# Optimization experiments

Measured on AMD Instinct MI355X. Metric: run time of the kernel, lower is better.

The kernel has to match this reference:

```python
import jax, jax.numpy as jnp
import numpy as np

EPS = 1e-9  # Dice BatchNormalization epsilon


def dice(x, alpha):
    # Keras BatchNormalization(axis=-1, center=False, scale=False) in training
    # mode: normalize over all axes except the last using batch statistics.
    mean = jnp.mean(x, axis=(0, 1), keepdims=True)
    var = jnp.var(x, axis=(0, 1), keepdims=True)
    x_normed = (x - mean) * jax.lax.rsqrt(var + EPS)
    p = jax.nn.sigmoid(x_normed)
    return alpha * (1.0 - p) * x + p * x


def setup_inputs() -> dict:
    key = jax.random.key(0)
    ks = jax.random.split(key, 11)
    B, T, D = 512, 2048, 20
    keys_ = jax.random.normal(ks[0], (B, T, D), dtype=jnp.float32)
    query = jax.random.normal(ks[1], (B, 1, D), dtype=jnp.float32)
    mask = jax.random.randint(ks[2], (B, T), 0, 2) > 0
    # DNN tower weights: hidden dims 80 -> 32 -> 16, attention head 16 -> 1
    W0 = jax.random.normal(ks[3], (80, 32), dtype=jnp.float32) * 0.1
    b0 = jax.random.normal(ks[4], (32,), dtype=jnp.float32) * 0.1
    a0 = jax.random.normal(ks[5], (32,), dtype=jnp.float32) * 0.1
    W1 = jax.random.normal(ks[6], (32, 16), dtype=jnp.float32) * 0.1
    b1 = jax.random.normal(ks[7], (16,), dtype=jnp.float32) * 0.1
    a1 = jax.random.normal(ks[8], (16,), dtype=jnp.float32) * 0.1
    wk = jax.random.normal(ks[9], (16, 1), dtype=jnp.float32) * 0.1
    bk = jax.random.normal(ks[10], (1,), dtype=jnp.float32) * 0.1
    return {"keys": keys_, "query": query, "mask": mask,
            "W0": W0, "b0": b0, "a0": a0,
            "W1": W1, "b1": b1, "a1": a1,
            "wk": wk, "bk": bk}


def reference(keys, query, mask, W0, b0, a0, W1, b1, a1, wk, bk):
    B, T, D = keys.shape
    # repeat query along the key/time axis: [B,1,D] -> [B,T,D]
    queries = jnp.broadcast_to(query, (B, T, D))
    # local-activation features: [B,T,4D] = [B,T,80]
    att = jnp.concatenate([queries, keys, queries - keys, queries * keys], axis=-1)
    # DNN tower with Dice activations (dropout is identity at inference)
    h = dice(att @ W0 + b0, a0)   # [B,T,32]
    h = dice(h @ W1 + b1, a1)     # [B,T,16]
    score = h @ wk + bk           # [B,T,1]
    outputs = jnp.transpose(score, (0, 2, 1))  # [B,1,T]
    # NOTE: the original code computes the masked scores into self.outputs but
    # then (weight_normalization=False, return_score=False) overwrites it with
    # matmul(outputs, keys) using the UNMASKED scores -- we reproduce that.
    return jnp.matmul(outputs, keys)  # [B,1,D]
```

## Files before the change

kernel.cpp:

```cpp
#include <hip/hip_runtime.h>
#include <hip/hip_cooperative_groups.h>

namespace cg = cooperative_groups;


#define BB 512
#define TT 2048
#define DD 20
#define C0 32
#define C1 16

#define NTH 256
#define NPOS 4
#define POSB (NTH * NPOS)
#define NROUND (TT / POSB)
#define NSLOT 8

#define WS_P1 0
#define WS_P2 512
#define WS_ZERO_N 768
#define WS_BLOB 896
#define BLOB_J 24
#define BLOB_B (C0 * BLOB_J)

#define PIN(x) asm volatile("" : "+v"(x))
#define AGLOAD(p) \
    __hip_atomic_load((p), __ATOMIC_RELAXED, __HIP_MEMORY_SCOPE_AGENT)

__device__ __forceinline__ float fast_sigmoid(float x) {
    return __builtin_amdgcn_rcpf(1.0f + __expf(-x));
}

__device__ __forceinline__ void load_krow(const float* __restrict__ row,
                                          float* kk) {
    const float4* kr = (const float4*)row;
    float4 a = kr[0], b = kr[1], c = kr[2], d = kr[3], e = kr[4];
    kk[0] = a.x; kk[1] = a.y; kk[2] = a.z; kk[3] = a.w;
    kk[4] = b.x; kk[5] = b.y; kk[6] = b.z; kk[7] = b.w;
    kk[8] = c.x; kk[9] = c.y; kk[10] = c.z; kk[11] = c.w;
    kk[12] = d.x; kk[13] = d.y; kk[14] = d.z; kk[15] = d.w;
    kk[16] = e.x; kk[17] = e.y; kk[18] = e.z; kk[19] = e.w;
}

__global__ void prep_kernel(const float* __restrict__ query,
                            const float* __restrict__ W0,
                            const float* __restrict__ b0,
                            float* __restrict__ blob) {
    const int b = blockIdx.x * 2 + (threadIdx.x >> 5);
    const int j = threadIdx.x & 31;
    float cj = b0[j];
    float* dst = blob + (size_t)b * BLOB_B + j * BLOB_J;
#pragma unroll
    for (int d = 0; d < DD; ++d) {
        float w_q = W0[d * C0 + j];
        float w_k = W0[(DD + d) * C0 + j];
        float w_d = W0[(2 * DD + d) * C0 + j];
        float w_p = W0[(3 * DD + d) * C0 + j];
        float qd = query[b * DD + d];
        dst[d] = w_k - w_d + qd * w_p;
        cj = fmaf(qd, w_q + w_d, cj);
    }
    dst[20] = cj;
}

#define LOAD_AND_PIN_KEYS(r)                                                 \
    float kk[NPOS][DD];                                                      \
    _Pragma("unroll") for (int pp = 0; pp < NPOS; ++pp)                      \
        load_krow(kbase + (size_t)((r)*POSB + tid + pp * NTH) * DD, kk[pp]); \
    _Pragma("unroll") for (int pp = 0; pp < NPOS; ++pp)                      \
        _Pragma("unroll") for (int d = 0; d < DD; ++d) PIN(kk[pp][d]);

#define TOWER_JLOOP()                                                        \
    _Pragma("unroll 1") for (int j = 0; j < C0; ++j) {                       \
        const float* wr = bA + j * BLOB_J;                                   \
        const float* ur = W1 + j * C1;                                       \
        const float cj = wr[20];                                             \
        const float2 ss = lss0[j];                                           \
        const float al = a0[j];                                              \
        const float nal = 1.0f - al;                                         \
        float h[NPOS];                                                       \
        _Pragma("unroll") for (int pp = 0; pp < NPOS; ++pp) {                \
            float hh = cj;                                                   \
            _Pragma("unroll") for (int d = 0; d < DD; ++d)                   \
                hh = fmaf(kk[pp][d], wr[d], hh);                             \
            h[pp] = hh;                                                      \
        }                                                                    \
        _Pragma("unroll") for (int pp = 0; pp < NPOS; ++pp) {                \
            float pr = fast_sigmoid(fmaf(h[pp], ss.x, ss.y));                \
            float h0d = h[pp] * fmaf(pr, nal, al);                           \
            _Pragma("unroll") for (int c = 0; c < C1; ++c)                   \
                h1[pp][c] = fmaf(h0d, ur[c], h1[pp][c]);                     \
        }                                                                    \
    }

__device__ __forceinline__ void phase1_body(int b, int tid, int lane,
                                            const float* __restrict__ bA,
                                            const float* __restrict__ kbase,
                                            float* __restrict__ ws) {
    float s[C0], q[C0];
#pragma unroll
    for (int j = 0; j < C0; ++j) { s[j] = 0.f; q[j] = 0.f; }
#pragma unroll 1
    for (int r = 0; r < NROUND; ++r) {
        LOAD_AND_PIN_KEYS(r)
#pragma unroll
        for (int j = 0; j < C0; ++j) {
            const float* wr = bA + j * BLOB_J;
            const float cj = wr[20];
            float sv = 0.f, qv = 0.f;
#pragma unroll
            for (int pp = 0; pp < NPOS; ++pp) {
                float hh = cj;
#pragma unroll
                for (int d = 0; d < DD; ++d) hh = fmaf(kk[pp][d], wr[d], hh);
                sv += hh;
                qv = fmaf(hh, hh, qv);
            }
            s[j] += sv;
            q[j] += qv;
        }
    }
    float redv = 0.f;
#pragma unroll
    for (int v = 0; v < 2 * C0; ++v) {
        float val = (v < C0) ? s[v] : q[v - C0];
#pragma unroll
        for (int o = 32; o >= 1; o >>= 1) val += __shfl_xor(val, o);
        if (lane == v) redv = val;
    }
    atomicAdd(&ws[WS_P1 + (b & (NSLOT - 1)) * (2 * C0) + lane], redv);
}

__device__ __forceinline__ void finalize0(int tid, float* __restrict__ ws,
                                          float2* __restrict__ lss0) {
    if (tid < C0) {
        float sv = 0.f, qv = 0.f;
#pragma unroll
        for (int k = 0; k < NSLOT; ++k) {
            sv += AGLOAD(&ws[WS_P1 + k * (2 * C0) + tid]);
            qv += AGLOAD(&ws[WS_P1 + k * (2 * C0) + C0 + tid]);
        }
        const float invN = 1.0f / (float)(BB * TT);
        float mean = sv * invN;
        float var = qv * invN - mean * mean;
        float sc = rsqrtf(var + 1e-9f);
        lss0[tid] = make_float2(sc, -mean * sc);
    }
}

__device__ __forceinline__ void phase2_body(
    int b, int tid, int lane, const float* __restrict__ bA,
    const float* __restrict__ kbase, const float* __restrict__ a0,
    const float* __restrict__ W1, const float* __restrict__ b1,
    const float2* __restrict__ lss0, float* __restrict__ ws) {
    float s1[C1], q1[C1];
#pragma unroll
    for (int c = 0; c < C1; ++c) { s1[c] = 0.f; q1[c] = 0.f; }
#pragma unroll 1
    for (int r = 0; r < NROUND; ++r) {
        LOAD_AND_PIN_KEYS(r)
        float h1[NPOS][C1];
#pragma unroll
        for (int pp = 0; pp < NPOS; ++pp)
#pragma unroll
            for (int c = 0; c < C1; ++c) h1[pp][c] = 0.f;
        TOWER_JLOOP()
#pragma unroll
        for (int c = 0; c < C1; ++c) {
            float bc = b1[c];
#pragma unroll
            for (int pp = 0; pp < NPOS; ++pp) {
                float v = h1[pp][c] + bc;
                s1[c] += v;
                q1[c] = fmaf(v, v, q1[c]);
            }
        }
    }
    float redv = 0.f;
#pragma unroll
    for (int v = 0; v < 2 * C1; ++v) {
        float val = (v < C1) ? s1[v] : q1[v - C1];
#pragma unroll
        for (int o = 32; o >= 1; o >>= 1) val += __shfl_xor(val, o);
        if (lane == v) redv = val;
    }
    if (lane < 2 * C1)
        atomicAdd(&ws[WS_P2 + (b & (NSLOT - 1)) * (2 * C1) + lane], redv);
}

__device__ __forceinline__ void finalize1(int tid, float* __restrict__ ws,
                                          const float* __restrict__ a1,
                                          const float* __restrict__ wk,
                                          float4* __restrict__ ld1v) {
    if (tid < C1) {
        float sv = 0.f, qv = 0.f;
#pragma unroll
        for (int k = 0; k < NSLOT; ++k) {
            sv += AGLOAD(&ws[WS_P2 + k * (2 * C1) + tid]);
            qv += AGLOAD(&ws[WS_P2 + k * (2 * C1) + C1 + tid]);
        }
        const float invN = 1.0f / (float)(BB * TT);
        float mean = sv * invN;
        float var = qv * invN - mean * mean;
        float sc = rsqrtf(var + 1e-9f);
        ld1v[tid] = make_float4(sc, -mean * sc, a1[tid], wk[tid]);
    }
}

__device__ __forceinline__ void phase3_body(
    int b, int tid, int lane, int wave, const float* __restrict__ bA,
    const float* __restrict__ kbase, const float* __restrict__ a0,
    const float* __restrict__ W1, const float* __restrict__ b1,
    const float* __restrict__ bk, const float2* __restrict__ lss0,
    const float4* __restrict__ ld1v, float (*red)[DD],
    float* __restrict__ out) {
    const float bkv = bk[0];
    float oacc[DD];
#pragma unroll
    for (int d = 0; d < DD; ++d) oacc[d] = 0.f;
#pragma unroll 1
    for (int r = 0; r < NROUND; ++r) {
        LOAD_AND_PIN_KEYS(r)
        float h1[NPOS][C1];
#pragma unroll
        for (int pp = 0; pp < NPOS; ++pp)
#pragma unroll
            for (int c = 0; c < C1; ++c) h1[pp][c] = 0.f;
        TOWER_JLOOP()
#pragma unroll
        for (int pp = 0; pp < NPOS; ++pp) {
            float score = bkv;
#pragma unroll
            for (int c = 0; c < C1; ++c) {
                float v = h1[pp][c] + b1[c];
                float4 dv = ld1v[c];
                float pr = fast_sigmoid(fmaf(v, dv.x, dv.y));
                float hd = v * fmaf(pr, 1.0f - dv.z, dv.z);
                score = fmaf(hd, dv.w, score);
            }
#pragma unroll
            for (int d = 0; d < DD; ++d)
                oacc[d] = fmaf(score, kk[pp][d], oacc[d]);
        }
    }
    float redv = 0.f;
#pragma unroll
    for (int v = 0; v < DD; ++v) {
        float val = oacc[v];
#pragma unroll
        for (int o = 32; o >= 1; o >>= 1) val += __shfl_xor(val, o);
        if (lane == v) redv = val;
    }
    if (lane < DD) red[wave][lane] = redv;
    __syncthreads();
    if (tid < DD)
        out[b * DD + tid] =
            red[0][tid] + red[1][tid] + red[2][tid] + red[3][tid];
}

__global__ __launch_bounds__(NTH, 2) void fused_kernel(
    const float* __restrict__ keys, const float* __restrict__ blob,
    const float* __restrict__ a0, const float* __restrict__ W1,
    const float* __restrict__ b1, const float* __restrict__ a1,
    const float* __restrict__ wk, const float* __restrict__ bk,
    float* __restrict__ ws, float* __restrict__ out) {
    const int b = blockIdx.x;
    const int tid = threadIdx.x, wave = tid >> 6, lane = tid & 63;
    const float* bA = blob + (size_t)b * BLOB_B;
    const float* kbase = keys + (size_t)b * TT * DD;

    __shared__ float2 lss0[C0];
    __shared__ float4 ld1v[C1];
    __shared__ float red[4][DD];

    phase1_body(b, tid, lane, bA, kbase, ws);
    cg::this_grid().sync();
    finalize0(tid, ws, lss0);
    __syncthreads();
    phase2_body(b, tid, lane, bA, kbase, a0, W1, b1, lss0, ws);
    cg::this_grid().sync();
    finalize1(tid, ws, a1, wk, ld1v);
    __syncthreads();
    phase3_body(b, tid, lane, wave, bA, kbase, a0, W1, b1, bk, lss0, ld1v,
                red, out);
}

__global__ __launch_bounds__(NTH, 2) void pass1_kernel(
    const float* __restrict__ keys, const float* __restrict__ blob,
    float* __restrict__ ws) {
    const int b = blockIdx.x;
    const int tid = threadIdx.x, lane = tid & 63;
    phase1_body(b, tid, lane, blob + (size_t)b * BLOB_B,
                keys + (size_t)b * TT * DD, ws);
}

__global__ __launch_bounds__(NTH, 2) void pass2_kernel(
    const float* __restrict__ keys, const float* __restrict__ blob,
    const float* __restrict__ a0, const float* __restrict__ W1,
    const float* __restrict__ b1, float* __restrict__ ws) {
    const int b = blockIdx.x;
    const int tid = threadIdx.x, lane = tid & 63;
    __shared__ float2 lss0[C0];
    finalize0(tid, ws, lss0);
    __syncthreads();
    phase2_body(b, tid, lane, blob + (size_t)b * BLOB_B,
                keys + (size_t)b * TT * DD, a0, W1, b1, lss0, ws);
}

__global__ __launch_bounds__(NTH, 2) void pass3_kernel(
    const float* __restrict__ keys, const float* __restrict__ blob,
    const float* __restrict__ a0, const float* __restrict__ W1,
    const float* __restrict__ b1, const float* __restrict__ a1,
    const float* __restrict__ wk, const float* __restrict__ bk,
    float* __restrict__ ws, float* __restrict__ out) {
    const int b = blockIdx.x;
    const int tid = threadIdx.x, wave = tid >> 6, lane = tid & 63;
    __shared__ float2 lss0[C0];
    __shared__ float4 ld1v[C1];
    __shared__ float red[4][DD];
    finalize0(tid, ws, lss0);
    finalize1(tid, ws, a1, wk, ld1v);
    __syncthreads();
    phase3_body(b, tid, lane, wave, blob + (size_t)b * BLOB_B,
                keys + (size_t)b * TT * DD, a0, W1, b1, bk, lss0, ld1v, red,
                out);
}

extern "C" void kernel_launch(void* const* d_in, const int* in_sizes, int n_in,
                              void* d_out, int out_size, void* d_ws,
                              size_t ws_size, hipStream_t stream) {
    const float* keys = (const float*)d_in[0];
    const float* query = (const float*)d_in[1];
    const float* W0 = (const float*)d_in[3];
    const float* b0 = (const float*)d_in[4];
    const float* a0 = (const float*)d_in[5];
    const float* W1 = (const float*)d_in[6];
    const float* b1 = (const float*)d_in[7];
    const float* a1 = (const float*)d_in[8];
    const float* wk = (const float*)d_in[9];
    const float* bk = (const float*)d_in[10];
    float* out = (float*)d_out;
    float* ws = (float*)d_ws;
    float* blob = ws + WS_BLOB;
    const float* blobc = blob;

    hipMemsetAsync(ws, 0, WS_ZERO_N * sizeof(float), stream);
    prep_kernel<<<BB / 2, 64, 0, stream>>>(query, W0, b0, blob);

    static int use_coop = -1;
    if (use_coop < 0) {
        int nb = 0, ncu = 0;
        hipError_t e1 = hipOccupancyMaxActiveBlocksPerMultiprocessor(
            &nb, (const void*)fused_kernel, NTH, 0);
        hipDeviceProp_t prop;
        hipError_t e2 = hipGetDeviceProperties(&prop, 0);
        if (e2 == hipSuccess) ncu = prop.multiProcessorCount;
        use_coop = (e1 == hipSuccess && e2 == hipSuccess && nb * ncu >= BB)
                       ? 1
                       : 0;
    }

    if (use_coop) {
        void* args[] = {(void*)&keys, (void*)&blobc, (void*)&a0, (void*)&W1,
                        (void*)&b1,   (void*)&a1,    (void*)&wk, (void*)&bk,
                        (void*)&ws,   (void*)&out};
        hipError_t e = hipLaunchCooperativeKernel(
            (const void*)fused_kernel, dim3(BB), dim3(NTH), args, 0, stream);
        if (e != hipSuccess) use_coop = 0;
    }
    if (!use_coop) {
        pass1_kernel<<<BB, NTH, 0, stream>>>(keys, blob, ws);
        pass2_kernel<<<BB, NTH, 0, stream>>>(keys, blob, a0, W1, b1, ws);
        pass3_kernel<<<BB, NTH, 0, stream>>>(keys, blob, a0, W1, b1, a1, wk,
                                             bk, ws, out);
    }
}
```

Measured before the change: 274.0 us.

## Split each batch across two blocks and raise occupancy to four blocks per CU

Each batch row's 2048 time steps are now split into two 1024-step chunks handled by separate blocks. The grid doubles, per-thread positions drop from 4 to 2, and launch bounds go from 2 to 4 blocks per CU. Because two blocks now contribute to each output row, the final write becomes an atomicAdd. Zeroing of the output and workspace moves into the prep kernel in place of the separate memset. The goal is more concurrent waves to hide memory latency and a lighter register load per thread. The cost is more atomics, a larger cooperative grid to synchronise, and tighter register limits that could cause spills.

```diff
diff --git a/kernel.cpp b/kernel.cpp
--- a/kernel.cpp
+++ b/kernel.cpp
@@ -11,9 +11,12 @@
 #define C1 16
 
 #define NTH 256
-#define NPOS 4
+#define NPOS 2
 #define POSB (NTH * NPOS)
-#define NROUND (TT / POSB)
+#define CHUNK 1024
+#define NROUND (CHUNK / POSB)
+#define NBLK (TT / CHUNK)
+#define GRID (BB * NBLK)
 #define NSLOT 8
 
 #define WS_P1 0
@@ -45,9 +48,14 @@
 __global__ void prep_kernel(const float* __restrict__ query,
                             const float* __restrict__ W0,
                             const float* __restrict__ b0,
-                            float* __restrict__ blob) {
+                            float* __restrict__ blob, float* __restrict__ ws,
+                            float* __restrict__ out) {
     const int b = blockIdx.x * 2 + (threadIdx.x >> 5);
     const int j = threadIdx.x & 31;
+    if (blockIdx.x == 0) {
+        for (int i = threadIdx.x; i < WS_ZERO_N; i += 64) ws[i] = 0.f;
+    }
+    if (j < DD) out[b * DD + j] = 0.f;
     float cj = b0[j];
     float* dst = blob + (size_t)b * BLOB_B + j * BLOB_J;
 #pragma unroll
@@ -93,7 +101,7 @@
         }                                                                    \
     }
 
-__device__ __forceinline__ void phase1_body(int b, int tid, int lane,
+__device__ __forceinline__ void phase1_body(int slot, int tid, int lane,
                                             const float* __restrict__ bA,
                                             const float* __restrict__ kbase,
                                             float* __restrict__ ws) {
@@ -128,7 +136,7 @@
         for (int o = 32; o >= 1; o >>= 1) val += __shfl_xor(val, o);
         if (lane == v) redv = val;
     }
-    atomicAdd(&ws[WS_P1 + (b & (NSLOT - 1)) * (2 * C0) + lane], redv);
+    atomicAdd(&ws[WS_P1 + slot * (2 * C0) + lane], redv);
 }
 
 __device__ __forceinline__ void finalize0(int tid, float* __restrict__ ws,
@@ -149,7 +157,7 @@
 }
 
 __device__ __forceinline__ void phase2_body(
-    int b, int tid, int lane, const float* __restrict__ bA,
+    int slot, int tid, int lane, const float* __restrict__ bA,
     const float* __restrict__ kbase, const float* __restrict__ a0,
     const float* __restrict__ W1, const float* __restrict__ b1,
     const float2* __restrict__ lss0, float* __restrict__ ws) {
@@ -185,7 +193,7 @@
         if (lane == v) redv = val;
     }
     if (lane < 2 * C1)
-        atomicAdd(&ws[WS_P2 + (b & (NSLOT - 1)) * (2 * C1) + lane], redv);
+        atomicAdd(&ws[WS_P2 + slot * (2 * C1) + lane], redv);
 }
 
 __device__ __forceinline__ void finalize1(int tid, float* __restrict__ ws,
@@ -208,7 +216,7 @@
 }
 
 __device__ __forceinline__ void phase3_body(
-    int b, int tid, int lane, int wave, const float* __restrict__ bA,
+    int batch, int tid, int lane, int wave, const float* __restrict__ bA,
     const float* __restrict__ kbase, const float* __restrict__ a0,
     const float* __restrict__ W1, const float* __restrict__ b1,
     const float* __restrict__ bk, const float2* __restrict__ lss0,
@@ -254,66 +262,70 @@
     if (lane < DD) red[wave][lane] = redv;
     __syncthreads();
     if (tid < DD)
-        out[b * DD + tid] =
-            red[0][tid] + red[1][tid] + red[2][tid] + red[3][tid];
-}
-
-__global__ __launch_bounds__(NTH, 2) void fused_kernel(
+        atomicAdd(&out[batch * DD + tid],
+                  red[0][tid] + red[1][tid] + red[2][tid] + red[3][tid]);
+}
+
+__global__ __launch_bounds__(NTH, 4) void fused_kernel(
     const float* __restrict__ keys, const float* __restrict__ blob,
     const float* __restrict__ a0, const float* __restrict__ W1,
     const float* __restrict__ b1, const float* __restrict__ a1,
     const float* __restrict__ wk, const float* __restrict__ bk,
     float* __restrict__ ws, float* __restrict__ out) {
-    const int b = blockIdx.x;
+    const int batch = blockIdx.x >> 1, chunk = blockIdx.x & 1;
+    const int slot = blockIdx.x & (NSLOT - 1);
     const int tid = threadIdx.x, wave = tid >> 6, lane = tid & 63;
-    const float* bA = blob + (size_t)b * BLOB_B;
-    const float* kbase = keys + (size_t)b * TT * DD;
+    const float* bA = blob + (size_t)batch * BLOB_B;
+    const float* kbase = keys + ((size_t)batch * TT + chunk * CHUNK) * DD;
 
     __shared__ float2 lss0[C0];
     __shared__ float4 ld1v[C1];
     __shared__ float red[4][DD];
 
-    phase1_body(b, tid, lane, bA, kbase, ws);
+    phase1_body(slot, tid, lane, bA, kbase, ws);
     cg::this_grid().sync();
     finalize0(tid, ws, lss0);
     __syncthreads();
-    phase2_body(b, tid, lane, bA, kbase, a0, W1, b1, lss0, ws);
+    phase2_body(slot, tid, lane, bA, kbase, a0, W1, b1, lss0, ws);
     cg::this_grid().sync();
     finalize1(tid, ws, a1, wk, ld1v);
     __syncthreads();
-    phase3_body(b, tid, lane, wave, bA, kbase, a0, W1, b1, bk, lss0, ld1v,
-                red, out);
-}
-
-__global__ __launch_bounds__(NTH, 2) void pass1_kernel(
+    phase3_body(batch, tid, lane, wave, bA, kbase, a0, W1, b1, bk, lss0,
+                ld1v, red, out);
+}
+
+__global__ __launch_bounds__(NTH, 4) void pass1_kernel(
     const float* __restrict__ keys, const float* __restrict__ blob,
     float* __restrict__ ws) {
-    const int b = blockIdx.x;
+    const int batch = blockIdx.x >> 1, chunk = blockIdx.x & 1;
     const int tid = threadIdx.x, lane = tid & 63;
-    phase1_body(b, tid, lane, blob + (size_t)b * BLOB_B,
-                keys + (size_t)b * TT * DD, ws);
-}
-
-__global__ __launch_bounds__(NTH, 2) void pass2_kernel(
+    phase1_body(blockIdx.x & (NSLOT - 1), tid, lane,
+                blob + (size_t)batch * BLOB_B,
+                keys + ((size_t)batch * TT + chunk * CHUNK) * DD, ws);
+}
+
+__global__ __launch_bounds__(NTH, 4) void pass2_kernel(
     const float* __restrict__ keys, const float* __restrict__ blob,
     const float* __restrict__ a0, const float* __restrict__ W1,
     const float* __restrict__ b1, float* __restrict__ ws) {
-    const int b = blockIdx.x;
+    const int batch = blockIdx.x >> 1, chunk = blockIdx.x & 1;
     const int tid = threadIdx.x, lane = tid & 63;
     __shared__ float2 lss0[C0];
     finalize0(tid, ws, lss0);
     __syncthreads();
-    phase2_body(b, tid, lane, blob + (size_t)b * BLOB_B,
-                keys + (size_t)b * TT * DD, a0, W1, b1, lss0, ws);
-}
-
-__global__ __launch_bounds__(NTH, 2) void pass3_kernel(
+    phase2_body(blockIdx.x & (NSLOT - 1), tid, lane,
+                blob + (size_t)batch * BLOB_B,
+                keys + ((size_t)batch * TT + chunk * CHUNK) * DD, a0, W1, b1,
+                lss0, ws);
+}
+
+__global__ __launch_bounds__(NTH, 4) void pass3_kernel(
     const float* __restrict__ keys, const float* __restrict__ blob,
     const float* __restrict__ a0, const float* __restrict__ W1,
     const float* __restrict__ b1, const float* __restrict__ a1,
     const float* __restrict__ wk, const float* __restrict__ bk,
     float* __restrict__ ws, float* __restrict__ out) {
-    const int b = blockIdx.x;
+    const int batch = blockIdx.x >> 1, chunk = blockIdx.x & 1;
     const int tid = threadIdx.x, wave = tid >> 6, lane = tid & 63;
     __shared__ float2 lss0[C0];
     __shared__ float4 ld1v[C1];
@@ -321,9 +333,9 @@
     finalize0(tid, ws, lss0);
     finalize1(tid, ws, a1, wk, ld1v);
     __syncthreads();
-    phase3_body(b, tid, lane, wave, blob + (size_t)b * BLOB_B,
-                keys + (size_t)b * TT * DD, a0, W1, b1, bk, lss0, ld1v, red,
-                out);
+    phase3_body(batch, tid, lane, wave, blob + (size_t)batch * BLOB_B,
+                keys + ((size_t)batch * TT + chunk * CHUNK) * DD, a0, W1, b1,
+                bk, lss0, ld1v, red, out);
 }
 
 extern "C" void kernel_launch(void* const* d_in, const int* in_sizes, int n_in,
@@ -344,8 +356,7 @@
     float* blob = ws + WS_BLOB;
     const float* blobc = blob;
 
-    hipMemsetAsync(ws, 0, WS_ZERO_N * sizeof(float), stream);
-    prep_kernel<<<BB / 2, 64, 0, stream>>>(query, W0, b0, blob);
+    prep_kernel<<<BB / 2, 64, 0, stream>>>(query, W0, b0, blob, ws, out);
 
     static int use_coop = -1;
     if (use_coop < 0) {
@@ -355,7 +366,7 @@
         hipDeviceProp_t prop;
         hipError_t e2 = hipGetDeviceProperties(&prop, 0);
         if (e2 == hipSuccess) ncu = prop.multiProcessorCount;
-        use_coop = (e1 == hipSuccess && e2 == hipSuccess && nb * ncu >= BB)
+        use_coop = (e1 == hipSuccess && e2 == hipSuccess && nb * ncu >= GRID)
                        ? 1
                        : 0;
     }
@@ -365,13 +376,14 @@
                         (void*)&b1,   (void*)&a1,    (void*)&wk, (void*)&bk,
                         (void*)&ws,   (void*)&out};
         hipError_t e = hipLaunchCooperativeKernel(
-            (const void*)fused_kernel, dim3(BB), dim3(NTH), args, 0, stream);
+            (const void*)fused_kernel, dim3(GRID), dim3(NTH), args, 0,
+            stream);
         if (e != hipSuccess) use_coop = 0;
     }
     if (!use_coop) {
-        pass1_kernel<<<BB, NTH, 0, stream>>>(keys, blob, ws);
-        pass2_kernel<<<BB, NTH, 0, stream>>>(keys, blob, a0, W1, b1, ws);
-        pass3_kernel<<<BB, NTH, 0, stream>>>(keys, blob, a0, W1, b1, a1, wk,
-                                             bk, ws, out);
-    }
-}
+        pass1_kernel<<<GRID, NTH, 0, stream>>>(keys, blob, ws);
+        pass2_kernel<<<GRID, NTH, 0, stream>>>(keys, blob, a0, W1, b1, ws);
+        pass3_kernel<<<GRID, NTH, 0, stream>>>(keys, blob, a0, W1, b1, a1, wk,
+                                               bk, ws, out);
+    }
+}
```

Result: slower. 289.7 us (+5.7%).
